# Performance work log

Hardware: AMD Instinct MI355X
Metric: run time of the kernel (lower is better)

## Reference

```python
import jax, jax.numpy as jnp
import numpy as np

RANGES = {"measure": 256, "beat": 16, "position": 128, "duration": 128, "pitch": 256,
          "instrument": 129, "velocity": 128, "key_sign": 24, "time_sign": 48, "tempo": 49}
R_TOTAL = sum(RANGES.values())  # 1162
NUMERATORS = jnp.array([1, 2, 3, 4, 5, 6, 7, 8, 9, 10, 12, 16], dtype=jnp.int32)
TOT_NUM = 12
NEG = jnp.float32(-1e9)


def _prefix_gather(x, axis=1):
    # value at position i becomes the cumulative value at index min(i+1, S-1):
    # reproduces the tf mask `range(S) <= idx+1` (prefix up to i+1 inclusive).
    S = x.shape[axis]
    idx = jnp.minimum(jnp.arange(S) + 1, S - 1)
    return jnp.take(x, idx, axis=axis)


def _present_mask(song, dtype_id, feat, R):
    # occ[b,i,v] = True iff some token j<=i+1 has type dtype_id and song[b,j,feat]==v
    # (vectorized form of tensor_scatter_nd_max over a prefix, via one-hot + cummax)
    match = song[..., 0] == dtype_id                       # [B,S]
    onehot = (song[..., feat][..., None] == jnp.arange(R)) & match[..., None]
    cum = jax.lax.cummax(onehot.astype(jnp.int32), axis=1)
    return _prefix_gather(cum, 1).astype(bool)             # [B,S,R]


def _has_any(song, dtype_id):
    match = (song[..., 0] == dtype_id).astype(jnp.int32)
    return _prefix_gather(jax.lax.cummax(match, axis=1), 1).astype(bool)  # [B,S]


def _last_value(song, dtype_id, feat):
    # song[b, argmax_j(match*j) , feat] over the prefix j<=i+1; tf argmax of all
    # zeros returns 0, reproduced by where(match, j, 0) + cummax.
    match = song[..., 0] == dtype_id
    j = jnp.arange(song.shape[1])
    last_idx = _prefix_gather(jax.lax.cummax(jnp.where(match, j, 0), axis=1), 1)
    return jnp.take_along_axis(song[..., feat], last_idx, axis=1)  # [B,S]


def _forward(song, chosen_type, scores):
    B, S, _ = song.shape
    Rm, Rb = RANGES["measure"], RANGES["beat"]
    ar_m = jnp.arange(RANGES["measure"]); ar_b = jnp.arange(RANGES["beat"])
    ar_p = jnp.arange(RANGES["position"])
    ar_ks = jnp.arange(RANGES["key_sign"]); ar_ts = jnp.arange(RANGES["time_sign"])
    ar_tp = jnp.arange(RANGES["tempo"])
    t = chosen_type[..., None]  # [B,S,1]

    inst_present = _present_mask(song, 1, 6, RANGES["instrument"])  # [B,S,129]
    has_inst = inst_present.any(-1, keepdims=True)

    last_ks = _last_value(song, 4, 8);  oh_ks = last_ks[..., None] == ar_ks
    last_ts = _last_value(song, 5, 9);  oh_ts = last_ts[..., None] == ar_ts
    last_tp = _last_value(song, 6, 10); oh_tp = last_tp[..., None] == ar_tp
    has_ks = _has_any(song, 4)[..., None]
    has_ts = _has_any(song, 5)[..., None]

    # ---- chosen_type == 3 (note-like token) ----
    min_measure = song[..., 1]
    pred_m = jnp.argmax(scores[..., :Rm], axis=-1).astype(jnp.int32)
    c1 = pred_m == min_measure
    min_beat = jnp.where(c1, song[..., 2], 0)
    pred_b = jnp.argmax(scores[..., Rm:Rm + Rb], axis=-1).astype(jnp.int32)
    c2 = c1 & (pred_b == min_beat)
    min_pos = jnp.where(c2, song[..., 3], 0)
    max_beat = NUMERATORS[jnp.mod(last_ts, TOT_NUM)]  # get_max_beat_from_time_sign
    m3 = ar_m >= min_measure[..., None]
    b3 = (ar_b >= min_beat[..., None]) & (ar_b < max_beat[..., None])
    p3 = ar_p >= min_pos[..., None]

    # ---- chosen_type == 1 (instrument): forbid already-present instruments ----
    inst1 = jnp.where(has_inst, ~inst_present, True)

    # ---- chosen_type in 4..6 (key_sign / time_sign / tempo) ----
    min_m46 = jnp.where((song[..., 2] == 0) & (song[..., 3] == 0),
                        song[..., 1], song[..., 1] + 1)
    m46 = ar_m >= min_m46[..., None]
    ks4 = jnp.where(has_ks, ~oh_ks, True)
    ts5 = jnp.where(has_ts, ~oh_ts, True)
    tp6 = ~oh_tp

    is3 = t == 3
    measure_mask = jnp.where(is3, m3, jnp.where((t >= 4) & (t <= 6), m46, True))
    beat_mask = jnp.where(is3, b3, True)
    position_mask = jnp.where(is3, p3, True)
    duration_mask = jnp.ones((B, S, RANGES["duration"]), bool)
    pitch_mask = jnp.ones((B, S, RANGES["pitch"]), bool)
    instrument_mask = jnp.where(is3, inst_present, jnp.where(t == 1, inst1, True))
    velocity_mask = jnp.ones((B, S, RANGES["velocity"]), bool)
    key_sign_mask = jnp.where(is3, oh_ks, jnp.where(t == 4, ks4, True))
    time_sign_mask = jnp.where(is3, oh_ts, jnp.where(t == 5, ts5, True))
    tempo_mask = jnp.where(is3, oh_tp, jnp.where(t == 6, tp6, True))

    mask = jnp.concatenate([measure_mask, beat_mask, position_mask, duration_mask,
                            pitch_mask, instrument_mask, velocity_mask,
                            key_sign_mask, time_sign_mask, tempo_mask], axis=-1)
    return jnp.where(mask, scores, NEG)  # masked logits [B,S,R_TOTAL]


def setup_inputs() -> dict:
    key = jax.random.key(0)
    k_song, k_type, k_scores = jax.random.split(key, 3)
    B, S = 8, 2047  # SEQ_LEN-1 with SEQ_LEN=2048
    col_max = [8, RANGES["measure"], RANGES["beat"], RANGES["position"],
               RANGES["duration"], RANGES["pitch"], RANGES["instrument"],
               RANGES["velocity"], RANGES["key_sign"], RANGES["time_sign"],
               RANGES["tempo"]]
    kcols = jax.random.split(k_song, 11)
    song = jnp.stack([jax.random.randint(kcols[c], (B, S), 0, col_max[c],
                                         dtype=jnp.int32) for c in range(11)], axis=-1)
    chosen_type = jax.random.randint(k_type, (B, S), 0, 8, dtype=jnp.int32)
    scores = jax.random.normal(k_scores, (B, S, R_TOTAL), dtype=jnp.float32)
    return {"song": song, "chosen_type": chosen_type, "scores": scores}


def reference(song, chosen_type, scores):
    return _forward(song, chosen_type, scores)
```

## Files before the change

### kernel.cpp

```cpp
#include <hip/hip_runtime.h>
#include <cstdint>
#include <cstddef>

#define S_LEN 2047
#define BATCH 8
#define R_TOT 1162
#define NCHUNK 8
#define NEGV (-1e9f)

#define CARRY_OFF 393024

__device__ __constant__ int d_numerators[12] = {1, 2, 3, 4, 5, 6, 7, 8, 9, 10, 12, 16};

__global__ __launch_bounds__(256) void scan_local(const int* __restrict__ song,
                                                  unsigned* __restrict__ local) {
    const int b = blockIdx.x >> 3;
    const int c = blockIdx.x & 7;
    const int tid = threadIdx.x;
    const int j = c * 256 + tid;
    __shared__ unsigned lds_f[3][256];
    __shared__ unsigned lds_inst[5][256];
    const unsigned HAS = 1u << 16;
    const long base = (long)b * S_LEN;

    unsigned e_f[3] = {0, 0, 0};
    unsigned e_inst[5] = {0, 0, 0, 0, 0};
    if (j < S_LEN) {
        const int* rj = song + (base + j) * 11;
        const int type = rj[0];
        if (type == 4)      e_f[0] = HAS | (unsigned)rj[8];
        else if (type == 5) e_f[1] = HAS | (unsigned)rj[9];
        else if (type == 6) e_f[2] = HAS | (unsigned)rj[10];
        else if (type == 1) { const int v = rj[6]; e_inst[v >> 5] = 1u << (v & 31); }
    }
#pragma unroll
    for (int w = 0; w < 3; w++) lds_f[w][tid] = e_f[w];
#pragma unroll
    for (int w = 0; w < 5; w++) lds_inst[w][tid] = e_inst[w];
    __syncthreads();

    for (int off = 1; off < 256; off <<= 1) {
        unsigned p_f[3] = {0, 0, 0};
        unsigned p_inst[5] = {0, 0, 0, 0, 0};
        if (tid >= off) {
#pragma unroll
            for (int w = 0; w < 3; w++) p_f[w] = lds_f[w][tid - off];
#pragma unroll
            for (int w = 0; w < 5; w++) p_inst[w] = lds_inst[w][tid - off];
        }
        __syncthreads();
        if (tid >= off) {
#pragma unroll
            for (int w = 0; w < 3; w++) {
                if (!(e_f[w] & HAS)) e_f[w] = p_f[w];
                lds_f[w][tid] = e_f[w];
            }
#pragma unroll
            for (int w = 0; w < 5; w++) {
                e_inst[w] |= p_inst[w];
                lds_inst[w][tid] = e_inst[w];
            }
        }
        __syncthreads();
    }

    if (j < S_LEN) {
        const unsigned w0 =
            (e_f[0] & 0xFFu) | ((e_f[1] & 0xFFu) << 8) | ((e_f[2] & 0xFFu) << 16) |
            (((e_f[0] >> 16) & 1u) << 24) | (((e_f[1] >> 16) & 1u) << 25) |
            (((e_f[2] >> 16) & 1u) << 26);
        unsigned* sp = local + (size_t)(base + j) * 6;
        sp[0] = w0;
#pragma unroll
        for (int w = 0; w < 5; w++) sp[1 + w] = e_inst[w];
    }
}

__global__ __launch_bounds__(64) void scan_carry(const int* __restrict__ song,
                                                 const unsigned* __restrict__ local,
                                                 unsigned* __restrict__ carry) {
    const int b = threadIdx.x;
    if (b >= BATCH) return;
    const int* r0 = song + (size_t)b * S_LEN * 11;
    unsigned cks = (unsigned)r0[8], cts = (unsigned)r0[9], ctp = (unsigned)r0[10];
    unsigned chas = 0;
    unsigned cinst[5] = {0, 0, 0, 0, 0};
    for (int c = 0; c < NCHUNK; c++) {
        unsigned* cp = carry + ((size_t)b * NCHUNK + c) * 6;
        cp[0] = (cks & 0xFFu) | ((cts & 0xFFu) << 8) | ((ctp & 0xFFu) << 16) | (chas << 24);
#pragma unroll
        for (int w = 0; w < 5; w++) cp[1 + w] = cinst[w];
        const int pos = min((c + 1) * 256, S_LEN) - 1;
        const unsigned* lp = local + ((size_t)b * S_LEN + pos) * 6;
        const unsigned a0 = lp[0];
        if ((a0 >> 24) & 1u) cks = a0 & 0xFFu;
        if ((a0 >> 25) & 1u) cts = (a0 >> 8) & 0xFFu;
        if ((a0 >> 26) & 1u) ctp = (a0 >> 16) & 0xFFu;
        chas |= (a0 >> 24) & 7u;
#pragma unroll
        for (int w = 0; w < 5; w++) cinst[w] |= lp[1 + w];
    }
}

__global__ __launch_bounds__(256) void mask_kernel(const int* __restrict__ song,
                                                   const int* __restrict__ ctype,
                                                   const float* __restrict__ scores,
                                                   const unsigned* __restrict__ local,
                                                   const unsigned* __restrict__ carry,
                                                   float* __restrict__ out) {
    const int row = blockIdx.x;
    const int tid = threadIdx.x;
    const int b = row / S_LEN;
    const int i = row - b * S_LEN;

    __shared__ float s_val[128];
    __shared__ int   s_idx[128];
    __shared__ float sb_val[8];
    __shared__ int   sb_idx[8];
    __shared__ int   s_info[10];
    __shared__ int   f_info[17];

    const size_t rbase = (size_t)row * R_TOT;
    const float2* s2 = (const float2*)(scores + rbase);
    float2* o2 = (float2*)(out + rbase);

    const float2 r0 = s2[tid];
    const float2 r1 = s2[tid + 256];
    float2 r2 = make_float2(0.f, 0.f);
    if (tid < 69) r2 = s2[tid + 512];

    if (tid < 128) {
        const bool sec = (r0.y > r0.x);
        s_val[tid] = sec ? r0.y : r0.x;
        s_idx[tid] = 2 * tid + (sec ? 1 : 0);
    } else if (tid < 136) {
        const bool sec = (r0.y > r0.x);
        sb_val[tid - 128] = sec ? r0.y : r0.x;
        sb_idx[tid - 128] = (2 * tid - 256) + (sec ? 1 : 0);
    } else if (tid < 142) {
        const int w = tid - 136;
        const int e = min(i + 1, S_LEN - 1);
        const unsigned lw = local[((size_t)b * S_LEN + e) * 6 + w];
        const unsigned cw = carry[((size_t)b * NCHUNK + (e >> 8)) * 6 + w];
        unsigned v;
        if (w == 0) {
            const unsigned ks = ((lw >> 24) & 1u) ? (lw & 0xFFu) : (cw & 0xFFu);
            const unsigned ts = ((lw >> 25) & 1u) ? ((lw >> 8) & 0xFFu) : ((cw >> 8) & 0xFFu);
            const unsigned tp = ((lw >> 26) & 1u) ? ((lw >> 16) & 0xFFu) : ((cw >> 16) & 0xFFu);
            const unsigned hks = ((lw >> 24) | (cw >> 24)) & 1u;
            const unsigned hts = ((lw >> 25) | (cw >> 25)) & 1u;
            v = ks | (ts << 8) | (tp << 16) | (hks << 24) | (hts << 25);
        } else {
            v = lw | cw;
        }
        s_info[w] = (int)v;
    } else if (tid < 146) {
        const int* srow = song + (size_t)row * 11;
        if (tid == 142) s_info[6] = srow[1];
        if (tid == 143) s_info[7] = srow[2];
        if (tid == 144) s_info[8] = srow[3];
        if (tid == 145) s_info[9] = ctype[row];
    }
    __syncthreads();

    for (int s = 64; s > 0; s >>= 1) {
        if (tid < s) {
            if (s_val[tid + s] > s_val[tid]) {
                s_val[tid] = s_val[tid + s];
                s_idx[tid] = s_idx[tid + s];
            }
        }
        __syncthreads();
    }

    if (tid == 0) {
        const int pred_m = s_idx[0];
        float bv = sb_val[0];
        int pred_b = sb_idx[0];
#pragma unroll
        for (int q = 1; q < 8; q++) {
            if (sb_val[q] > bv) { bv = sb_val[q]; pred_b = sb_idx[q]; }
        }
        const unsigned pack = (unsigned)s_info[0];
        const int song1 = s_info[6], song2 = s_info[7], song3 = s_info[8];
        const int t = s_info[9];
        const bool c1 = (pred_m == song1);
        const int min_beat = c1 ? song2 : 0;
        const bool c2 = c1 && (pred_b == min_beat);
        const int min_pos = c2 ? song3 : 0;
        const int last_ks = pack & 0xFF;
        const int last_ts = (pack >> 8) & 0xFF;
        const int last_tp = (pack >> 16) & 0xFF;
        f_info[0] = t;
        f_info[1] = song1;
        f_info[2] = min_beat;
        f_info[3] = min_pos;
        f_info[4] = (song2 == 0 && song3 == 0) ? song1 : song1 + 1;
        f_info[5] = d_numerators[last_ts % 12];
        f_info[6] = last_ks;
        f_info[7] = last_ts;
        f_info[8] = last_tp;
        f_info[9]  = (int)((pack >> 24) & 1u);
        f_info[10] = (int)((pack >> 25) & 1u);
        const unsigned u = (unsigned)s_info[1] | (unsigned)s_info[2] | (unsigned)s_info[3] |
                           (unsigned)s_info[4] | (unsigned)s_info[5];
        f_info[11] = (u != 0u);
        f_info[12] = s_info[1]; f_info[13] = s_info[2]; f_info[14] = s_info[3];
        f_info[15] = s_info[4]; f_info[16] = s_info[5];
    }
    __syncthreads();

    const int t = f_info[0];
    const int min_measure = f_info[1], min_beat = f_info[2], min_pos = f_info[3];
    const int min_m46 = f_info[4], max_beat = f_info[5];
    const int last_ks = f_info[6], last_ts = f_info[7], last_tp = f_info[8];
    const bool has_ks = f_info[9] != 0, has_ts = f_info[10] != 0, has_inst = f_info[11] != 0;
    unsigned inst[5];
#pragma unroll
    for (int w = 0; w < 5; w++) inst[w] = (unsigned)f_info[12 + w];
    const bool is3 = (t == 3);
    const bool is46 = (t >= 4) && (t <= 6);

    auto maskf = [&](int col) -> bool {
        if (col < 256) {
            if (is3) return col >= min_measure;
            if (is46) return col >= min_m46;
            return true;
        } else if (col < 272) {
            if (!is3) return true;
            const int v = col - 256;
            return (v >= min_beat) && (v < max_beat);
        } else if (col < 400) {
            return is3 ? ((col - 272) >= min_pos) : true;
        } else if (col < 784) {
            return true;
        } else if (col < 913) {
            const int v = col - 784;
            const bool pres = ((inst[v >> 5] >> (v & 31)) & 1u) != 0u;
            if (is3) return pres;
            if (t == 1) return has_inst ? !pres : true;
            return true;
        } else if (col < 1041) {
            return true;
        } else if (col < 1065) {
            const int v = col - 1041;
            if (is3) return v == last_ks;
            if (t == 4) return has_ks ? (v != last_ks) : true;
            return true;
        } else if (col < 1113) {
            const int v = col - 1065;
            if (is3) return v == last_ts;
            if (t == 5) return has_ts ? (v != last_ts) : true;
            return true;
        } else {
            const int v = col - 1113;
            if (is3) return v == last_tp;
            if (t == 6) return v != last_tp;
            return true;
        }
    };

    float2 w;
    int c = 2 * tid;
    w.x = maskf(c)     ? r0.x : NEGV;
    w.y = maskf(c + 1) ? r0.y : NEGV;
    o2[tid] = w;

    c = 512 + 2 * tid;
    w.x = maskf(c)     ? r1.x : NEGV;
    w.y = maskf(c + 1) ? r1.y : NEGV;
    o2[tid + 256] = w;

    if (tid < 69) {
        c = 1024 + 2 * tid;
        w.x = maskf(c)     ? r2.x : NEGV;
        w.y = maskf(c + 1) ? r2.y : NEGV;
        o2[tid + 512] = w;
    }
}

extern "C" void kernel_launch(void* const* d_in, const int* in_sizes, int n_in,
                              void* d_out, int out_size, void* d_ws, size_t ws_size,
                              hipStream_t stream) {
    const int* song = (const int*)d_in[0];
    const int* ctype = (const int*)d_in[1];
    const float* scores = (const float*)d_in[2];
    float* out = (float*)d_out;
    unsigned* local = (unsigned*)d_ws;
    unsigned* carry = (unsigned*)((char*)d_ws + CARRY_OFF);

    scan_local<<<BATCH * NCHUNK, 256, 0, stream>>>(song, local);
    scan_carry<<<1, 64, 0, stream>>>(song, local, carry);
    mask_kernel<<<BATCH * S_LEN, 256, 0, stream>>>(song, ctype, scores, local, carry, out);
}
```

Measured before the change: 155.2 us.

## Process row pairs per block with float4 IO and early-exit copy path

The mask kernel now handles two rows per 512-thread block, loading and storing the pair's scores as float4 since two rows of 1162 floats are 16-byte aligned together. When both rows have a chosen type that never masks (0, 2, 7), the block copies scores straight through and skips the argmax reduction and the scan lookups. This halves the block count and widens memory transactions, but mask evaluation now reads per-row parameters from shared memory on every column and needs a per-element row select.

```diff
diff --git a/kernel.cpp b/kernel.cpp
--- a/kernel.cpp
+++ b/kernel.cpp
@@ -7,6 +7,8 @@
 #define R_TOT 1162
 #define NCHUNK 8
 #define NEGV (-1e9f)
+#define NROWS (BATCH * S_LEN)
+#define NPAIR (NROWS / 2)
 
 #define CARRY_OFF 393024
 
@@ -102,43 +104,62 @@
     }
 }
 
-__global__ __launch_bounds__(256) void mask_kernel(const int* __restrict__ song,
-                                                   const int* __restrict__ ctype,
-                                                   const float* __restrict__ scores,
-                                                   const unsigned* __restrict__ local,
-                                                   const unsigned* __restrict__ carry,
-                                                   float* __restrict__ out) {
-    const int row = blockIdx.x;
+__global__ __launch_bounds__(512) void mask_pair(const int* __restrict__ song,
+                                                 const int* __restrict__ ctype,
+                                                 const float* __restrict__ scores,
+                                                 const unsigned* __restrict__ local,
+                                                 const unsigned* __restrict__ carry,
+                                                 float* __restrict__ out) {
+    const int pair = blockIdx.x;
     const int tid = threadIdx.x;
+    const int half = tid >> 8;
+    const int th = tid & 255;
+    const int row = pair * 2 + half;
+
+    __shared__ float s_val[2][128];
+    __shared__ int   s_idx[2][128];
+    __shared__ float sb_val[2][8];
+    __shared__ int   sb_idx[2][8];
+    __shared__ int   s_info[2][10];
+    __shared__ int   f_info[2][17];
+
+    const size_t pbase = (size_t)pair * (2 * R_TOT);
+    const float4* s4 = (const float4*)(scores + pbase);
+    float4* o4 = (float4*)(out + pbase);
+
+    const int tA = ctype[pair * 2];
+    const int tB = ctype[pair * 2 + 1];
+    const bool copyA = (tA == 0 || tA == 2 || tA == 7);
+    const bool copyB = (tB == 0 || tB == 2 || tB == 7);
+
+    float4 v0 = s4[tid];
+    float4 v1 = make_float4(0.f, 0.f, 0.f, 0.f);
+    if (tid < 69) v1 = s4[512 + tid];
+
+    if (copyA && copyB) {
+        o4[tid] = v0;
+        if (tid < 69) o4[512 + tid] = v1;
+        return;
+    }
+
     const int b = row / S_LEN;
     const int i = row - b * S_LEN;
-
-    __shared__ float s_val[128];
-    __shared__ int   s_idx[128];
-    __shared__ float sb_val[8];
-    __shared__ int   sb_idx[8];
-    __shared__ int   s_info[10];
-    __shared__ int   f_info[17];
-
     const size_t rbase = (size_t)row * R_TOT;
     const float2* s2 = (const float2*)(scores + rbase);
-    float2* o2 = (float2*)(out + rbase);
-
-    const float2 r0 = s2[tid];
-    const float2 r1 = s2[tid + 256];
-    float2 r2 = make_float2(0.f, 0.f);
-    if (tid < 69) r2 = s2[tid + 512];
-
-    if (tid < 128) {
-        const bool sec = (r0.y > r0.x);
-        s_val[tid] = sec ? r0.y : r0.x;
-        s_idx[tid] = 2 * tid + (sec ? 1 : 0);
-    } else if (tid < 136) {
-        const bool sec = (r0.y > r0.x);
-        sb_val[tid - 128] = sec ? r0.y : r0.x;
-        sb_idx[tid - 128] = (2 * tid - 256) + (sec ? 1 : 0);
-    } else if (tid < 142) {
-        const int w = tid - 136;
+
+    if (th < 136) {
+        const float2 r0 = s2[th];
+        if (th < 128) {
+            const bool sec = (r0.y > r0.x);
+            s_val[half][th] = sec ? r0.y : r0.x;
+            s_idx[half][th] = 2 * th + (sec ? 1 : 0);
+        } else {
+            const bool sec = (r0.y > r0.x);
+            sb_val[half][th - 128] = sec ? r0.y : r0.x;
+            sb_idx[half][th - 128] = (2 * th - 256) + (sec ? 1 : 0);
+        }
+    } else if (th < 142) {
+        const int w = th - 136;
         const int e = min(i + 1, S_LEN - 1);
         const unsigned lw = local[((size_t)b * S_LEN + e) * 6 + w];
         const unsigned cw = carry[((size_t)b * NCHUNK + (e >> 8)) * 6 + w];
@@ -153,37 +174,37 @@
         } else {
             v = lw | cw;
         }
-        s_info[w] = (int)v;
-    } else if (tid < 146) {
+        s_info[half][w] = (int)v;
+    } else if (th < 146) {
         const int* srow = song + (size_t)row * 11;
-        if (tid == 142) s_info[6] = srow[1];
-        if (tid == 143) s_info[7] = srow[2];
-        if (tid == 144) s_info[8] = srow[3];
-        if (tid == 145) s_info[9] = ctype[row];
+        if (th == 142) s_info[half][6] = srow[1];
+        if (th == 143) s_info[half][7] = srow[2];
+        if (th == 144) s_info[half][8] = srow[3];
+        if (th == 145) s_info[half][9] = ctype[row];
     }
     __syncthreads();
 
     for (int s = 64; s > 0; s >>= 1) {
-        if (tid < s) {
-            if (s_val[tid + s] > s_val[tid]) {
-                s_val[tid] = s_val[tid + s];
-                s_idx[tid] = s_idx[tid + s];
+        if (th < s) {
+            if (s_val[half][th + s] > s_val[half][th]) {
+                s_val[half][th] = s_val[half][th + s];
+                s_idx[half][th] = s_idx[half][th + s];
             }
         }
         __syncthreads();
     }
 
-    if (tid == 0) {
-        const int pred_m = s_idx[0];
-        float bv = sb_val[0];
-        int pred_b = sb_idx[0];
+    if (th == 0) {
+        const int pred_m = s_idx[half][0];
+        float bv = sb_val[half][0];
+        int pred_b = sb_idx[half][0];
 #pragma unroll
         for (int q = 1; q < 8; q++) {
-            if (sb_val[q] > bv) { bv = sb_val[q]; pred_b = sb_idx[q]; }
-        }
-        const unsigned pack = (unsigned)s_info[0];
-        const int song1 = s_info[6], song2 = s_info[7], song3 = s_info[8];
-        const int t = s_info[9];
+            if (sb_val[half][q] > bv) { bv = sb_val[half][q]; pred_b = sb_idx[half][q]; }
+        }
+        const unsigned pack = (unsigned)s_info[half][0];
+        const int song1 = s_info[half][6], song2 = s_info[half][7], song3 = s_info[half][8];
+        const int t = s_info[half][9];
         const bool c1 = (pred_m == song1);
         const int min_beat = c1 ? song2 : 0;
         const bool c2 = c1 && (pred_b == min_beat);
@@ -191,91 +212,89 @@
         const int last_ks = pack & 0xFF;
         const int last_ts = (pack >> 8) & 0xFF;
         const int last_tp = (pack >> 16) & 0xFF;
-        f_info[0] = t;
-        f_info[1] = song1;
-        f_info[2] = min_beat;
-        f_info[3] = min_pos;
-        f_info[4] = (song2 == 0 && song3 == 0) ? song1 : song1 + 1;
-        f_info[5] = d_numerators[last_ts % 12];
-        f_info[6] = last_ks;
-        f_info[7] = last_ts;
-        f_info[8] = last_tp;
-        f_info[9]  = (int)((pack >> 24) & 1u);
-        f_info[10] = (int)((pack >> 25) & 1u);
-        const unsigned u = (unsigned)s_info[1] | (unsigned)s_info[2] | (unsigned)s_info[3] |
-                           (unsigned)s_info[4] | (unsigned)s_info[5];
-        f_info[11] = (u != 0u);
-        f_info[12] = s_info[1]; f_info[13] = s_info[2]; f_info[14] = s_info[3];
-        f_info[15] = s_info[4]; f_info[16] = s_info[5];
+        f_info[half][0] = t;
+        f_info[half][1] = song1;
+        f_info[half][2] = min_beat;
+        f_info[half][3] = min_pos;
+        f_info[half][4] = (song2 == 0 && song3 == 0) ? song1 : song1 + 1;
+        f_info[half][5] = d_numerators[last_ts % 12];
+        f_info[half][6] = last_ks;
+        f_info[half][7] = last_ts;
+        f_info[half][8] = last_tp;
+        f_info[half][9]  = (int)((pack >> 24) & 1u);
+        f_info[half][10] = (int)((pack >> 25) & 1u);
+        const unsigned u = (unsigned)s_info[half][1] | (unsigned)s_info[half][2] |
+                           (unsigned)s_info[half][3] | (unsigned)s_info[half][4] |
+                           (unsigned)s_info[half][5];
+        f_info[half][11] = (u != 0u);
+        f_info[half][12] = s_info[half][1]; f_info[half][13] = s_info[half][2];
+        f_info[half][14] = s_info[half][3]; f_info[half][15] = s_info[half][4];
+        f_info[half][16] = s_info[half][5];
     }
     __syncthreads();
 
-    const int t = f_info[0];
-    const int min_measure = f_info[1], min_beat = f_info[2], min_pos = f_info[3];
-    const int min_m46 = f_info[4], max_beat = f_info[5];
-    const int last_ks = f_info[6], last_ts = f_info[7], last_tp = f_info[8];
-    const bool has_ks = f_info[9] != 0, has_ts = f_info[10] != 0, has_inst = f_info[11] != 0;
-    unsigned inst[5];
-#pragma unroll
-    for (int w = 0; w < 5; w++) inst[w] = (unsigned)f_info[12 + w];
-    const bool is3 = (t == 3);
-    const bool is46 = (t >= 4) && (t <= 6);
-
-    auto maskf = [&](int col) -> bool {
+    auto maskf = [&](int col, int r) -> bool {
+        const int t = f_info[r][0];
+        const bool is3 = (t == 3);
         if (col < 256) {
-            if (is3) return col >= min_measure;
-            if (is46) return col >= min_m46;
+            if (is3) return col >= f_info[r][1];
+            if (t >= 4 && t <= 6) return col >= f_info[r][4];
             return true;
         } else if (col < 272) {
             if (!is3) return true;
             const int v = col - 256;
-            return (v >= min_beat) && (v < max_beat);
+            return (v >= f_info[r][2]) && (v < f_info[r][5]);
         } else if (col < 400) {
-            return is3 ? ((col - 272) >= min_pos) : true;
+            return is3 ? ((col - 272) >= f_info[r][3]) : true;
         } else if (col < 784) {
             return true;
         } else if (col < 913) {
             const int v = col - 784;
-            const bool pres = ((inst[v >> 5] >> (v & 31)) & 1u) != 0u;
+            const bool pres = (((unsigned)f_info[r][12 + (v >> 5)] >> (v & 31)) & 1u) != 0u;
             if (is3) return pres;
-            if (t == 1) return has_inst ? !pres : true;
+            if (t == 1) return f_info[r][11] ? !pres : true;
             return true;
         } else if (col < 1041) {
             return true;
         } else if (col < 1065) {
             const int v = col - 1041;
-            if (is3) return v == last_ks;
-            if (t == 4) return has_ks ? (v != last_ks) : true;
+            if (is3) return v == f_info[r][6];
+            if (t == 4) return f_info[r][9] ? (v != f_info[r][6]) : true;
             return true;
         } else if (col < 1113) {
             const int v = col - 1065;
-            if (is3) return v == last_ts;
-            if (t == 5) return has_ts ? (v != last_ts) : true;
+            if (is3) return v == f_info[r][7];
+            if (t == 5) return f_info[r][10] ? (v != f_info[r][7]) : true;
             return true;
         } else {
             const int v = col - 1113;
-            if (is3) return v == last_tp;
-            if (t == 6) return v != last_tp;
+            if (is3) return v == f_info[r][8];
+            if (t == 6) return v != f_info[r][8];
             return true;
         }
     };
 
-    float2 w;
-    int c = 2 * tid;
-    w.x = maskf(c)     ? r0.x : NEGV;
-    w.y = maskf(c + 1) ? r0.y : NEGV;
-    o2[tid] = w;
-
-    c = 512 + 2 * tid;
-    w.x = maskf(c)     ? r1.x : NEGV;
-    w.y = maskf(c + 1) ? r1.y : NEGV;
-    o2[tid + 256] = w;
-
+    {
+        const int e = 4 * tid;
+        float4 w;
+        int col = e;       int r = (col >= R_TOT); col -= r ? R_TOT : 0;
+        w.x = maskf(col, r) ? v0.x : NEGV;
+        col = e + 1;       r = (col >= R_TOT); col -= r ? R_TOT : 0;
+        w.y = maskf(col, r) ? v0.y : NEGV;
+        col = e + 2;       r = (col >= R_TOT); col -= r ? R_TOT : 0;
+        w.z = maskf(col, r) ? v0.z : NEGV;
+        col = e + 3;       r = (col >= R_TOT); col -= r ? R_TOT : 0;
+        w.w = maskf(col, r) ? v0.w : NEGV;
+        o4[tid] = w;
+    }
     if (tid < 69) {
-        c = 1024 + 2 * tid;
-        w.x = maskf(c)     ? r2.x : NEGV;
-        w.y = maskf(c + 1) ? r2.y : NEGV;
-        o2[tid + 512] = w;
+        const int e = 4 * (512 + tid);
+        float4 w;
+        w.x = maskf(e     - R_TOT, 1) ? v1.x : NEGV;
+        w.y = maskf(e + 1 - R_TOT, 1) ? v1.y : NEGV;
+        w.z = maskf(e + 2 - R_TOT, 1) ? v1.z : NEGV;
+        w.w = maskf(e + 3 - R_TOT, 1) ? v1.w : NEGV;
+        o4[512 + tid] = w;
     }
 }
 
@@ -291,5 +310,5 @@
 
     scan_local<<<BATCH * NCHUNK, 256, 0, stream>>>(song, local);
     scan_carry<<<1, 64, 0, stream>>>(song, local, carry);
-    mask_kernel<<<BATCH * S_LEN, 256, 0, stream>>>(song, ctype, scores, local, carry, out);
+    mask_pair<<<NPAIR, 512, 0, stream>>>(song, ctype, scores, local, carry, out);
 }
```

Measured after the change: 169.1 us. 8.9% more time.
